# Optimization experiments

Measured on AMD Instinct MI355X. Metric: run time of the kernel, lower is better.

The kernel has to match this reference:

```python
import jax, jax.numpy as jnp
import numpy as np

N_NODES = 100000
N_EDGES = 1600000
IN_C = 128
HID_C = 64
HEADS = 2
OUT_C = 40
NEG_SLOPE = 0.2  # PyG GATConv default


def setup_inputs() -> dict:
    key = jax.random.key(0)
    ks = jax.random.split(key, 10)
    x = jax.random.normal(ks[0], (N_NODES, IN_C), dtype=jnp.float32)
    edge_index = jax.random.randint(ks[1], (2, N_EDGES), 0, N_NODES, dtype=jnp.int32)
    # layer 1 params: Linear(in, heads*hid), att_src/att_dst [heads, hid], bias [heads*hid]
    s1 = 1.0 / np.sqrt(IN_C)
    W1 = jax.random.uniform(ks[2], (IN_C, HEADS * HID_C), minval=-s1, maxval=s1, dtype=jnp.float32)
    att_src1 = jax.random.normal(ks[3], (HEADS, HID_C), dtype=jnp.float32) * 0.1
    att_dst1 = jax.random.normal(ks[4], (HEADS, HID_C), dtype=jnp.float32) * 0.1
    b1 = jnp.zeros((HEADS * HID_C,), dtype=jnp.float32)
    # layer 2 params: Linear(heads*hid, out), heads=1, concat=False
    s2 = 1.0 / np.sqrt(HEADS * HID_C)
    W2 = jax.random.uniform(ks[5], (HEADS * HID_C, OUT_C), minval=-s2, maxval=s2, dtype=jnp.float32)
    att_src2 = jax.random.normal(ks[6], (1, OUT_C), dtype=jnp.float32) * 0.1
    att_dst2 = jax.random.normal(ks[7], (1, OUT_C), dtype=jnp.float32) * 0.1
    b2 = jnp.zeros((OUT_C,), dtype=jnp.float32)
    return {"x": x, "edge_index": edge_index, "W1": W1, "att_src1": att_src1,
            "att_dst1": att_dst1, "b1": b1, "W2": W2, "att_src2": att_src2,
            "att_dst2": att_dst2, "b2": b2}


def _gat_conv(x, src, dst, n, W, a_src, a_dst):
    # x: [N, F_in]; W: [F_in, H*C]; a_src/a_dst: [H, C]
    H, C = a_src.shape
    h = (x @ W).reshape(n, H, C)                       # [N, H, C]
    alpha_src = jnp.einsum('nhc,hc->nh', h, a_src)     # [N, H]
    alpha_dst = jnp.einsum('nhc,hc->nh', h, a_dst)
    e = alpha_src[src] + alpha_dst[dst]                # [E, H]
    e = jax.nn.leaky_relu(e, NEG_SLOPE)
    # numerically stable softmax over edges grouped by destination node
    m = jax.ops.segment_max(e, dst, num_segments=n)    # [N, H]
    ex = jnp.exp(e - m[dst])
    s = jax.ops.segment_sum(ex, dst, num_segments=n)
    coef = ex / (s[dst] + 1e-16)                       # [E, H]
    msg = h[src] * coef[:, :, None]                    # [E, H, C]
    return jax.ops.segment_sum(msg, dst, num_segments=n)  # [N, H, C]


def reference(x, edge_index, W1, att_src1, att_dst1, b1, W2, att_src2, att_dst2, b2):
    n = x.shape[0]
    # PyG GATConv adds self-loops by default
    loops = jnp.arange(n, dtype=edge_index.dtype)
    src = jnp.concatenate([edge_index[0], loops])
    dst = jnp.concatenate([edge_index[1], loops])
    # layer 1: heads=2, concat -> [N, H*C] + bias, then ELU
    h1 = _gat_conv(x, src, dst, n, W1, att_src1, att_dst1)
    h1 = h1.reshape(n, -1) + b1
    h1 = jax.nn.elu(h1)
    # layer 2: heads=1, concat=False -> mean over heads (=squeeze) + bias
    h2 = _gat_conv(h1, src, dst, n, W2, att_src2, att_dst2)
    h2 = h2.mean(axis=1) + b2
    return jax.nn.log_softmax(h2, axis=1)
```

## Files before the change

kernel.cpp:

```cpp
#include <hip/hip_runtime.h>
#include <hip/hip_fp16.h>
#include <math.h>

#define N_NODES 100000
#define N_EDGES 1600000
#define E_TOT   (N_EDGES + N_NODES)

#define NB     512
#define NPB    196
#define BCAP   4096
#define BIN_CH 4096
#define NBIN_WG ((E_TOT + BIN_CH - 1) / BIN_CH)

__device__ __forceinline__ float wexp(float v) {
    v = v > 0.f ? v : 0.2f * v;
    return __expf(v);
}

__global__ __launch_bounds__(256) void gemm1_k(
    const float* __restrict__ x, const float* __restrict__ W1,
    const float* __restrict__ as1, const float* __restrict__ ad1,
    __half* __restrict__ h1h, float* __restrict__ asrc, float* __restrict__ adst)
{
    __shared__ float xs[64][65];
    __shared__ float Wsh[64][128];
    const int t = threadIdx.x;
    const int nbase = blockIdx.x * 64;
    const int c4 = t & 31;
    const int ng = t >> 5;

    float acc[8][4];
#pragma unroll
    for (int i = 0; i < 8; ++i)
#pragma unroll
        for (int j = 0; j < 4; ++j) acc[i][j] = 0.f;

    for (int kt = 0; kt < 128; kt += 64) {
        __syncthreads();
        {
            int r = t >> 4;
            int c = (t & 15) * 4;
#pragma unroll
            for (int p = 0; p < 4; ++p) {
                int row = p * 16 + r;
                int gr = nbase + row; if (gr > N_NODES - 1) gr = N_NODES - 1;
                float4 v = *(const float4*)(x + (size_t)gr * 128 + kt + c);
                xs[row][c + 0] = v.x; xs[row][c + 1] = v.y;
                xs[row][c + 2] = v.z; xs[row][c + 3] = v.w;
            }
        }
        {
            int r = t >> 5;
            int c = (t & 31) * 4;
#pragma unroll
            for (int p = 0; p < 8; ++p) {
                int row = p * 8 + r;
                *(float4*)&Wsh[row][c] = *(const float4*)(W1 + (size_t)(kt + row) * 128 + c);
            }
        }
        __syncthreads();

#pragma unroll 4
        for (int k = 0; k < 64; ++k) {
            float4 w = *(const float4*)&Wsh[k][c4 * 4];
            float x0 = xs[ng * 8 + 0][k], x1 = xs[ng * 8 + 1][k];
            float x2 = xs[ng * 8 + 2][k], x3 = xs[ng * 8 + 3][k];
            float x4 = xs[ng * 8 + 4][k], x5 = xs[ng * 8 + 5][k];
            float x6 = xs[ng * 8 + 6][k], x7 = xs[ng * 8 + 7][k];
            acc[0][0] += x0 * w.x; acc[0][1] += x0 * w.y; acc[0][2] += x0 * w.z; acc[0][3] += x0 * w.w;
            acc[1][0] += x1 * w.x; acc[1][1] += x1 * w.y; acc[1][2] += x1 * w.z; acc[1][3] += x1 * w.w;
            acc[2][0] += x2 * w.x; acc[2][1] += x2 * w.y; acc[2][2] += x2 * w.z; acc[2][3] += x2 * w.w;
            acc[3][0] += x3 * w.x; acc[3][1] += x3 * w.y; acc[3][2] += x3 * w.z; acc[3][3] += x3 * w.w;
            acc[4][0] += x4 * w.x; acc[4][1] += x4 * w.y; acc[4][2] += x4 * w.z; acc[4][3] += x4 * w.w;
            acc[5][0] += x5 * w.x; acc[5][1] += x5 * w.y; acc[5][2] += x5 * w.z; acc[5][3] += x5 * w.w;
            acc[6][0] += x6 * w.x; acc[6][1] += x6 * w.y; acc[6][2] += x6 * w.z; acc[6][3] += x6 * w.w;
            acc[7][0] += x7 * w.x; acc[7][1] += x7 * w.y; acc[7][2] += x7 * w.z; acc[7][3] += x7 * w.w;
        }
    }

    float4 as4 = ((const float4*)as1)[c4];
    float4 ad4 = ((const float4*)ad1)[c4];
#pragma unroll
    for (int i = 0; i < 8; ++i) {
        int node = nbase + ng * 8 + i;
        float ax = acc[i][0], ay = acc[i][1], az = acc[i][2], aw = acc[i][3];
        if (node < N_NODES) {
            __half2* row = (__half2*)(h1h + (size_t)node * 128);
            row[2 * c4]     = __floats2half2_rn(ax, ay);
            row[2 * c4 + 1] = __floats2half2_rn(az, aw);
        }
        float ps = ax * as4.x + ay * as4.y + az * as4.z + aw * as4.w;
        float pd = ax * ad4.x + ay * ad4.y + az * ad4.z + aw * ad4.w;
#pragma unroll
        for (int off = 1; off < 16; off <<= 1) {
            ps += __shfl_xor(ps, off);
            pd += __shfl_xor(pd, off);
        }
        if ((t & 15) == 0 && node < N_NODES) {
            int h = c4 >> 4;
            asrc[node * 2 + h] = ps;
            adst[node * 2 + h] = pd;
        }
    }
}

__global__ __launch_bounds__(256) void bin_k(
    const int* __restrict__ ei, int* __restrict__ bcur, unsigned* __restrict__ bdata)
{
    __shared__ int hist[NB];
    __shared__ int base[NB];
    const int t = threadIdx.x;
    const int e0 = blockIdx.x * BIN_CH;
    const int n = min(BIN_CH, E_TOT - e0);

    for (int b = t; b < NB; b += 256) hist[b] = 0;
    __syncthreads();

    for (int i = t; i < n; i += 256) {
        int e = e0 + i;
        int d = (e < N_EDGES) ? ei[N_EDGES + e] : e - N_EDGES;
        atomicAdd(&hist[d / NPB], 1);
    }
    __syncthreads();

    for (int b = t; b < NB; b += 256) {
        int c = hist[b];
        base[b] = c ? atomicAdd(&bcur[b], c) : 0;
        hist[b] = 0;
    }
    __syncthreads();

    for (int i = t; i < n; i += 256) {
        int e = e0 + i;
        int s, d;
        if (e < N_EDGES) { s = ei[e]; d = ei[N_EDGES + e]; }
        else             { s = d = e - N_EDGES; }
        int b  = d / NPB;
        int dl = d - b * NPB;
        int pos = base[b] + atomicAdd(&hist[b], 1);
        if (pos < BCAP)
            bdata[(size_t)b * BCAP + pos] = (unsigned)s | ((unsigned)dl << 17);
    }
}

__global__ __launch_bounds__(512) void scanb_k(
    const int* __restrict__ bcur, int* __restrict__ bbase)
{
    __shared__ int a[NB], b_[NB];
    int t = threadIdx.x;
    int v = bcur[t];
    a[t] = v;
    __syncthreads();
    int* src = a; int* dst = b_;
    for (int off = 1; off < NB; off <<= 1) {
        dst[t] = (t >= off) ? src[t - off] + src[t] : src[t];
        __syncthreads();
        int* tmp = src; src = dst; dst = tmp;
    }
    bbase[t] = src[t] - v;
}

__global__ __launch_bounds__(256) void build_k(
    const unsigned* __restrict__ bdata, const int* __restrict__ bcur,
    const int* __restrict__ bbase, int* __restrict__ row_start,
    int* __restrict__ csr_src)
{
    __shared__ unsigned rec[BCAP];
    __shared__ int hist[256];
    __shared__ int excl[NPB];
    __shared__ int lcur[NPB];
    const int t = threadIdx.x;
    const int b = blockIdx.x;
    const int cnt = min(bcur[b], BCAP);
    const int bb = bbase[b];

    hist[t] = 0;
    if (t < NPB) lcur[t] = 0;
    __syncthreads();

    for (int i = t; i < cnt; i += 256) {
        unsigned r = bdata[(size_t)b * BCAP + i];
        rec[i] = r;
        atomicAdd(&hist[r >> 17], 1);
    }
    __syncthreads();

    int v = hist[t];
    __syncthreads();
    for (int off = 1; off < 256; off <<= 1) {
        int y = (t >= off) ? hist[t - off] : 0;
        __syncthreads();
        hist[t] += y;
        __syncthreads();
    }
    if (t < NPB) excl[t] = hist[t] - v;
    __syncthreads();

    int node = b * NPB + t;
    if (t < NPB && node <= N_NODES) row_start[node] = bb + excl[t];

    for (int i = t; i < cnt; i += 256) {
        unsigned r = rec[i];
        int dl = r >> 17;
        int s  = r & 0x1FFFF;
        int slot = atomicAdd(&lcur[dl], 1);
        csr_src[bb + excl[dl] + slot] = s;
    }
}

__global__ __launch_bounds__(256) void fagg1_k(
    const int* __restrict__ csr_src, const int* __restrict__ row_start,
    const float* __restrict__ asrc, const float* __restrict__ adst,
    const __half* __restrict__ h1h, const float* __restrict__ b1,
    __half* __restrict__ out1h)
{
    int node = blockIdx.x * 4 + (threadIdx.x >> 6);
    int L = threadIdx.x & 63;
    int h = L >> 5;
    int b = row_start[node], e = row_start[node + 1];
    const float* as_h = asrc + h;
    float ad = adst[node * 2 + h];
    const __half2* H = (const __half2*)h1h;

    float2 a0 = make_float2(0.f, 0.f), a1 = a0, a2 = a0, a3 = a0;
    float d0 = 0.f, d1 = 0.f, d2 = 0.f, d3 = 0.f;

    int j = b;
    for (; j + 3 < e; j += 4) {
        int s0 = csr_src[j], s1 = csr_src[j + 1], s2 = csr_src[j + 2], s3 = csr_src[j + 3];
        float w0 = wexp(as_h[s0 * 2] + ad);
        float w1 = wexp(as_h[s1 * 2] + ad);
        float w2 = wexp(as_h[s2 * 2] + ad);
        float w3 = wexp(as_h[s3 * 2] + ad);
        float2 x0 = __half22float2(H[(size_t)s0 * 64 + L]);
        float2 x1 = __half22float2(H[(size_t)s1 * 64 + L]);
        float2 x2 = __half22float2(H[(size_t)s2 * 64 + L]);
        float2 x3 = __half22float2(H[(size_t)s3 * 64 + L]);
        a0.x += w0 * x0.x; a0.y += w0 * x0.y; d0 += w0;
        a1.x += w1 * x1.x; a1.y += w1 * x1.y; d1 += w1;
        a2.x += w2 * x2.x; a2.y += w2 * x2.y; d2 += w2;
        a3.x += w3 * x3.x; a3.y += w3 * x3.y; d3 += w3;
    }
    for (; j < e; ++j) {
        int s = csr_src[j];
        float w = wexp(as_h[s * 2] + ad);
        float2 xv = __half22float2(H[(size_t)s * 64 + L]);
        a0.x += w * xv.x; a0.y += w * xv.y; d0 += w;
    }

    float inv = 1.f / (((d0 + d1) + (d2 + d3)) + 1e-16f);
    float2 bb = ((const float2*)b1)[L];
    float vx = (a0.x + a1.x + a2.x + a3.x) * inv + bb.x;
    float vy = (a0.y + a1.y + a2.y + a3.y) * inv + bb.y;
    vx = vx > 0.f ? vx : expm1f(vx);
    vy = vy > 0.f ? vy : expm1f(vy);
    ((__half2*)(out1h + (size_t)node * 128))[L] = __floats2half2_rn(vx, vy);
}

__global__ __launch_bounds__(256) void gemm2_k(
    const __half* __restrict__ in1h, const float* __restrict__ W2,
    const float* __restrict__ as2, const float* __restrict__ ad2,
    __half* __restrict__ h2h, float* __restrict__ asrc, float* __restrict__ adst)
{
    __shared__ float xs[64][65];
    __shared__ float Wsh[64][64];
    __shared__ float as_s[64], ad_s[64];
    const int t = threadIdx.x;
    const int nbase = blockIdx.x * 64;
    const int c4 = t & 15;
    const int ng = t >> 4;

    if (t < 64) {
        as_s[t] = (t < 40) ? as2[t] : 0.f;
        ad_s[t] = (t < 40) ? ad2[t] : 0.f;
    }

    float acc[4][4];
#pragma unroll
    for (int i = 0; i < 4; ++i)
#pragma unroll
        for (int j = 0; j < 4; ++j) acc[i][j] = 0.f;

    for (int kt = 0; kt < 128; kt += 64) {
        __syncthreads();
        {
            int r = t >> 4;
            int c = (t & 15) * 4;
#pragma unroll
            for (int p = 0; p < 4; ++p) {
                int row = p * 16 + r;
                int gr = nbase + row; if (gr > N_NODES - 1) gr = N_NODES - 1;
                const __half2* src = (const __half2*)(in1h + (size_t)gr * 128 + kt + c);
                float2 f01 = __half22float2(src[0]);
                float2 f23 = __half22float2(src[1]);
                xs[row][c + 0] = f01.x; xs[row][c + 1] = f01.y;
                xs[row][c + 2] = f23.x; xs[row][c + 3] = f23.y;
            }
        }
        for (int i = t; i < 4096; i += 256) {
            int k = i >> 6, c = i & 63;
            Wsh[k][c] = (c < 40) ? W2[(size_t)(kt + k) * 40 + c] : 0.f;
        }
        __syncthreads();

#pragma unroll 4
        for (int k = 0; k < 64; ++k) {
            float4 w = *(const float4*)&Wsh[k][c4 * 4];
            float x0 = xs[ng * 4 + 0][k], x1 = xs[ng * 4 + 1][k];
            float x2 = xs[ng * 4 + 2][k], x3 = xs[ng * 4 + 3][k];
            acc[0][0] += x0 * w.x; acc[0][1] += x0 * w.y; acc[0][2] += x0 * w.z; acc[0][3] += x0 * w.w;
            acc[1][0] += x1 * w.x; acc[1][1] += x1 * w.y; acc[1][2] += x1 * w.z; acc[1][3] += x1 * w.w;
            acc[2][0] += x2 * w.x; acc[2][1] += x2 * w.y; acc[2][2] += x2 * w.z; acc[2][3] += x2 * w.w;
            acc[3][0] += x3 * w.x; acc[3][1] += x3 * w.y; acc[3][2] += x3 * w.z; acc[3][3] += x3 * w.w;
        }
    }

    float4 as4 = *(const float4*)&as_s[c4 * 4];
    float4 ad4 = *(const float4*)&ad_s[c4 * 4];
#pragma unroll
    for (int i = 0; i < 4; ++i) {
        int node = nbase + ng * 4 + i;
        float ax = acc[i][0], ay = acc[i][1], az = acc[i][2], aw = acc[i][3];
        if (node < N_NODES) {
            __half2* row = (__half2*)(h2h + (size_t)node * 64);
            row[2 * c4]     = __floats2half2_rn(ax, ay);
            row[2 * c4 + 1] = __floats2half2_rn(az, aw);
        }
        float ps = ax * as4.x + ay * as4.y + az * as4.z + aw * as4.w;
        float pd = ax * ad4.x + ay * ad4.y + az * ad4.z + aw * ad4.w;
#pragma unroll
        for (int off = 1; off < 16; off <<= 1) {
            ps += __shfl_xor(ps, off);
            pd += __shfl_xor(pd, off);
        }
        if ((t & 15) == 0 && node < N_NODES) {
            asrc[node] = ps;
            adst[node] = pd;
        }
    }
}

__global__ __launch_bounds__(256) void fagg2_k(
    const int* __restrict__ csr_src, const int* __restrict__ row_start,
    const float* __restrict__ asrc, const float* __restrict__ adst,
    const __half* __restrict__ h2h, const float* __restrict__ b2,
    float* __restrict__ out)
{
    int node = blockIdx.x * 4 + (threadIdx.x >> 6);
    int L = threadIdx.x & 63;
    bool act = L < 40;
    int col = act ? L : 0;
    int b = row_start[node], e = row_start[node + 1];
    float ad = adst[node];

    float a0 = 0.f, a1 = 0.f, a2 = 0.f, a3 = 0.f;
    float d0 = 0.f, d1 = 0.f, d2 = 0.f, d3 = 0.f;

    int j = b;
    for (; j + 3 < e; j += 4) {
        int s0 = csr_src[j], s1 = csr_src[j + 1], s2 = csr_src[j + 2], s3 = csr_src[j + 3];
        float w0 = wexp(asrc[s0] + ad);
        float w1 = wexp(asrc[s1] + ad);
        float w2 = wexp(asrc[s2] + ad);
        float w3 = wexp(asrc[s3] + ad);
        float x0 = __half2float(h2h[(size_t)s0 * 64 + col]);
        float x1 = __half2float(h2h[(size_t)s1 * 64 + col]);
        float x2 = __half2float(h2h[(size_t)s2 * 64 + col]);
        float x3 = __half2float(h2h[(size_t)s3 * 64 + col]);
        a0 += w0 * x0; d0 += w0;
        a1 += w1 * x1; d1 += w1;
        a2 += w2 * x2; d2 += w2;
        a3 += w3 * x3; d3 += w3;
    }
    for (; j < e; ++j) {
        int s = csr_src[j];
        float w = wexp(asrc[s] + ad);
        float xv = __half2float(h2h[(size_t)s * 64 + col]);
        a0 += w * xv; d0 += w;
    }

    float den = (d0 + d1) + (d2 + d3);
    float acc = (a0 + a1) + (a2 + a3);
    float v = act ? acc / (den + 1e-16f) + b2[L] : -1e30f;
    float mx = v;
#pragma unroll
    for (int off = 32; off; off >>= 1) mx = fmaxf(mx, __shfl_xor(mx, off));
    float ex = act ? __expf(v - mx) : 0.f;
#pragma unroll
    for (int off = 32; off; off >>= 1) ex += __shfl_xor(ex, off);
    if (act) out[(size_t)node * 40 + L] = v - mx - logf(ex);
}

extern "C" void kernel_launch(void* const* d_in, const int* in_sizes, int n_in,
                              void* d_out, int out_size, void* d_ws, size_t ws_size,
                              hipStream_t stream)
{
    const float* x   = (const float*)d_in[0];
    const int*   ei  = (const int*)d_in[1];
    const float* W1  = (const float*)d_in[2];
    const float* as1 = (const float*)d_in[3];
    const float* ad1 = (const float*)d_in[4];
    const float* b1  = (const float*)d_in[5];
    const float* W2  = (const float*)d_in[6];
    const float* as2 = (const float*)d_in[7];
    const float* ad2 = (const float*)d_in[8];
    const float* b2  = (const float*)d_in[9];
    float* out = (float*)d_out;

    float* ws = (float*)d_ws;
    __half* h1h   = (__half*)ws;
    __half* out1h = (__half*)(ws + 6400000);
    float* asrc1 = ws + 19200000;
    float* adst1 = ws + 19400000;
    float* asrc2 = ws + 19600000;
    float* adst2 = ws + 19700000;
    int* bcur      = (int*)(ws + 19800000);
    int* bbase     = (int*)(ws + 19801000);
    int* row_start = (int*)(ws + 19802000);
    int* csr_src   = (int*)(ws + 19910000);
    unsigned* bdata = (unsigned*)(ws + 21700000);

    hipMemsetAsync(bcur, 0, NB * sizeof(int), stream);

    bin_k<<<NBIN_WG, 256, 0, stream>>>(ei, bcur, bdata);
    scanb_k<<<1, 512, 0, stream>>>(bcur, bbase);
    build_k<<<NB, 256, 0, stream>>>(bdata, bcur, bbase, row_start, csr_src);

    gemm1_k<<<1563, 256, 0, stream>>>(x, W1, as1, ad1, h1h, asrc1, adst1);
    fagg1_k<<<25000, 256, 0, stream>>>(csr_src, row_start, asrc1, adst1, h1h, b1, out1h);

    __half* h2h = h1h;
    gemm2_k<<<1563, 256, 0, stream>>>(out1h, W2, as2, ad2, h2h, asrc2, adst2);
    fagg2_k<<<25000, 256, 0, stream>>>(csr_src, row_start, asrc2, adst2, h2h, b2, out);
}
```

Measured before the change: 301.3 us.

## Precompute per-edge attention weights and denominators in separate edge kernels

Adds edge-weight kernels that compute the leaky-relu exp attention weight once per edge (and per head), store them in CSR order, and reduce per-node denominators. The aggregation kernels then read contiguous weights instead of gathering asrc and recomputing exp in every lane. This removes redundant per-lane exp and random asrc gathers, but adds two extra launches plus a write and re-read of the edge weight arrays. Workspace offsets are shifted to make room for the new buffers.

```diff
diff --git a/kernel.cpp b/kernel.cpp
--- a/kernel.cpp
+++ b/kernel.cpp
@@ -208,9 +208,54 @@
     }
 }
 
+__global__ __launch_bounds__(256) void edgew1_k(
+    const int* __restrict__ csr_src, const int* __restrict__ row_start,
+    const float2* __restrict__ asrc2, const float2* __restrict__ adst2,
+    float2* __restrict__ wn, float2* __restrict__ dsum)
+{
+    int node = blockIdx.x * 4 + (threadIdx.x >> 6);
+    int L = threadIdx.x & 63;
+    int b = row_start[node], e = row_start[node + 1];
+    float2 ad = adst2[node];
+    float s0 = 0.f, s1 = 0.f;
+    for (int j = b + L; j < e; j += 64) {
+        float2 av = asrc2[csr_src[j]];
+        float w0 = wexp(av.x + ad.x);
+        float w1 = wexp(av.y + ad.y);
+        wn[j] = make_float2(w0, w1);
+        s0 += w0; s1 += w1;
+    }
+#pragma unroll
+    for (int off = 32; off; off >>= 1) {
+        s0 += __shfl_xor(s0, off);
+        s1 += __shfl_xor(s1, off);
+    }
+    if (L == 0) dsum[node] = make_float2(s0, s1);
+}
+
+__global__ __launch_bounds__(256) void edgew2_k(
+    const int* __restrict__ csr_src, const int* __restrict__ row_start,
+    const float* __restrict__ asrc, const float* __restrict__ adst,
+    float* __restrict__ wn, float* __restrict__ dsum)
+{
+    int node = blockIdx.x * 4 + (threadIdx.x >> 6);
+    int L = threadIdx.x & 63;
+    int b = row_start[node], e = row_start[node + 1];
+    float ad = adst[node];
+    float s = 0.f;
+    for (int j = b + L; j < e; j += 64) {
+        float w = wexp(asrc[csr_src[j]] + ad);
+        wn[j] = w;
+        s += w;
+    }
+#pragma unroll
+    for (int off = 32; off; off >>= 1) s += __shfl_xor(s, off);
+    if (L == 0) dsum[node] = s;
+}
+
 __global__ __launch_bounds__(256) void fagg1_k(
     const int* __restrict__ csr_src, const int* __restrict__ row_start,
-    const float* __restrict__ asrc, const float* __restrict__ adst,
+    const float2* __restrict__ wn, const float2* __restrict__ dsum,
     const __half* __restrict__ h1h, const float* __restrict__ b1,
     __half* __restrict__ out1h)
 {
@@ -218,37 +263,37 @@
     int L = threadIdx.x & 63;
     int h = L >> 5;
     int b = row_start[node], e = row_start[node + 1];
-    const float* as_h = asrc + h;
-    float ad = adst[node * 2 + h];
     const __half2* H = (const __half2*)h1h;
 
     float2 a0 = make_float2(0.f, 0.f), a1 = a0, a2 = a0, a3 = a0;
-    float d0 = 0.f, d1 = 0.f, d2 = 0.f, d3 = 0.f;
 
     int j = b;
     for (; j + 3 < e; j += 4) {
         int s0 = csr_src[j], s1 = csr_src[j + 1], s2 = csr_src[j + 2], s3 = csr_src[j + 3];
-        float w0 = wexp(as_h[s0 * 2] + ad);
-        float w1 = wexp(as_h[s1 * 2] + ad);
-        float w2 = wexp(as_h[s2 * 2] + ad);
-        float w3 = wexp(as_h[s3 * 2] + ad);
+        float2 u0 = wn[j], u1 = wn[j + 1], u2 = wn[j + 2], u3 = wn[j + 3];
         float2 x0 = __half22float2(H[(size_t)s0 * 64 + L]);
         float2 x1 = __half22float2(H[(size_t)s1 * 64 + L]);
         float2 x2 = __half22float2(H[(size_t)s2 * 64 + L]);
         float2 x3 = __half22float2(H[(size_t)s3 * 64 + L]);
-        a0.x += w0 * x0.x; a0.y += w0 * x0.y; d0 += w0;
-        a1.x += w1 * x1.x; a1.y += w1 * x1.y; d1 += w1;
-        a2.x += w2 * x2.x; a2.y += w2 * x2.y; d2 += w2;
-        a3.x += w3 * x3.x; a3.y += w3 * x3.y; d3 += w3;
+        float w0 = h ? u0.y : u0.x;
+        float w1 = h ? u1.y : u1.x;
+        float w2 = h ? u2.y : u2.x;
+        float w3 = h ? u3.y : u3.x;
+        a0.x += w0 * x0.x; a0.y += w0 * x0.y;
+        a1.x += w1 * x1.x; a1.y += w1 * x1.y;
+        a2.x += w2 * x2.x; a2.y += w2 * x2.y;
+        a3.x += w3 * x3.x; a3.y += w3 * x3.y;
     }
     for (; j < e; ++j) {
         int s = csr_src[j];
-        float w = wexp(as_h[s * 2] + ad);
+        float2 u = wn[j];
+        float w = h ? u.y : u.x;
         float2 xv = __half22float2(H[(size_t)s * 64 + L]);
-        a0.x += w * xv.x; a0.y += w * xv.y; d0 += w;
-    }
-
-    float inv = 1.f / (((d0 + d1) + (d2 + d3)) + 1e-16f);
+        a0.x += w * xv.x; a0.y += w * xv.y;
+    }
+
+    float2 ds = dsum[node];
+    float inv = 1.f / ((h ? ds.y : ds.x) + 1e-16f);
     float2 bb = ((const float2*)b1)[L];
     float vx = (a0.x + a1.x + a2.x + a3.x) * inv + bb.x;
     float vy = (a0.y + a1.y + a2.y + a3.y) * inv + bb.y;
@@ -320,14 +365,14 @@
 #pragma unroll
     for (int i = 0; i < 4; ++i) {
         int node = nbase + ng * 4 + i;
-        float ax = acc[i][0], ay = acc[i][1], az = acc[i][2], aw = acc[i][3];
+        float axx = acc[i][0], ayy = acc[i][1], azz = acc[i][2], aww = acc[i][3];
         if (node < N_NODES) {
             __half2* row = (__half2*)(h2h + (size_t)node * 64);
-            row[2 * c4]     = __floats2half2_rn(ax, ay);
-            row[2 * c4 + 1] = __floats2half2_rn(az, aw);
-        }
-        float ps = ax * as4.x + ay * as4.y + az * as4.z + aw * as4.w;
-        float pd = ax * ad4.x + ay * ad4.y + az * ad4.z + aw * ad4.w;
+            row[2 * c4]     = __floats2half2_rn(axx, ayy);
+            row[2 * c4 + 1] = __floats2half2_rn(azz, aww);
+        }
+        float ps = axx * as4.x + ayy * as4.y + azz * as4.z + aww * as4.w;
+        float pd = axx * ad4.x + ayy * ad4.y + azz * ad4.z + aww * ad4.w;
 #pragma unroll
         for (int off = 1; off < 16; off <<= 1) {
             ps += __shfl_xor(ps, off);
@@ -342,7 +387,7 @@
 
 __global__ __launch_bounds__(256) void fagg2_k(
     const int* __restrict__ csr_src, const int* __restrict__ row_start,
-    const float* __restrict__ asrc, const float* __restrict__ adst,
+    const float* __restrict__ wn, const float* __restrict__ dsum,
     const __half* __restrict__ h2h, const float* __restrict__ b2,
     float* __restrict__ out)
 {
@@ -351,35 +396,30 @@
     bool act = L < 40;
     int col = act ? L : 0;
     int b = row_start[node], e = row_start[node + 1];
-    float ad = adst[node];
 
     float a0 = 0.f, a1 = 0.f, a2 = 0.f, a3 = 0.f;
-    float d0 = 0.f, d1 = 0.f, d2 = 0.f, d3 = 0.f;
 
     int j = b;
     for (; j + 3 < e; j += 4) {
         int s0 = csr_src[j], s1 = csr_src[j + 1], s2 = csr_src[j + 2], s3 = csr_src[j + 3];
-        float w0 = wexp(asrc[s0] + ad);
-        float w1 = wexp(asrc[s1] + ad);
-        float w2 = wexp(asrc[s2] + ad);
-        float w3 = wexp(asrc[s3] + ad);
+        float w0 = wn[j], w1 = wn[j + 1], w2 = wn[j + 2], w3 = wn[j + 3];
         float x0 = __half2float(h2h[(size_t)s0 * 64 + col]);
         float x1 = __half2float(h2h[(size_t)s1 * 64 + col]);
         float x2 = __half2float(h2h[(size_t)s2 * 64 + col]);
         float x3 = __half2float(h2h[(size_t)s3 * 64 + col]);
-        a0 += w0 * x0; d0 += w0;
-        a1 += w1 * x1; d1 += w1;
-        a2 += w2 * x2; d2 += w2;
-        a3 += w3 * x3; d3 += w3;
+        a0 += w0 * x0;
+        a1 += w1 * x1;
+        a2 += w2 * x2;
+        a3 += w3 * x3;
     }
     for (; j < e; ++j) {
         int s = csr_src[j];
-        float w = wexp(asrc[s] + ad);
+        float w = wn[j];
         float xv = __half2float(h2h[(size_t)s * 64 + col]);
-        a0 += w * xv; d0 += w;
-    }
-
-    float den = (d0 + d1) + (d2 + d3);
+        a0 += w * xv;
+    }
+
+    float den = dsum[node];
     float acc = (a0 + a1) + (a2 + a3);
     float v = act ? acc / (den + 1e-16f) + b2[L] : -1e30f;
     float mx = v;
@@ -414,11 +454,15 @@
     float* adst1 = ws + 19400000;
     float* asrc2 = ws + 19600000;
     float* adst2 = ws + 19700000;
-    int* bcur      = (int*)(ws + 19800000);
-    int* bbase     = (int*)(ws + 19801000);
-    int* row_start = (int*)(ws + 19802000);
-    int* csr_src   = (int*)(ws + 19910000);
-    unsigned* bdata = (unsigned*)(ws + 21700000);
+    float* dsum1 = ws + 19810000;
+    float* dsum2 = ws + 20010000;
+    int* bcur      = (int*)(ws + 20110000);
+    int* bbase     = (int*)(ws + 20111000);
+    int* row_start = (int*)(ws + 20112000);
+    int* csr_src   = (int*)(ws + 20220000);
+    unsigned* bdata = (unsigned*)(ws + 22000000);
+    float* wn1     = ws + 24100000;
+    float* wn2     = wn1;
 
     hipMemsetAsync(bcur, 0, NB * sizeof(int), stream);
 
@@ -427,9 +471,15 @@
     build_k<<<NB, 256, 0, stream>>>(bdata, bcur, bbase, row_start, csr_src);
 
     gemm1_k<<<1563, 256, 0, stream>>>(x, W1, as1, ad1, h1h, asrc1, adst1);
-    fagg1_k<<<25000, 256, 0, stream>>>(csr_src, row_start, asrc1, adst1, h1h, b1, out1h);
+    edgew1_k<<<25000, 256, 0, stream>>>(csr_src, row_start,
+                                        (const float2*)asrc1, (const float2*)adst1,
+                                        (float2*)wn1, (float2*)dsum1);
+    fagg1_k<<<25000, 256, 0, stream>>>(csr_src, row_start,
+                                       (const float2*)wn1, (const float2*)dsum1,
+                                       h1h, b1, out1h);
 
     __half* h2h = h1h;
     gemm2_k<<<1563, 256, 0, stream>>>(out1h, W2, as2, ad2, h2h, asrc2, adst2);
-    fagg2_k<<<25000, 256, 0, stream>>>(csr_src, row_start, asrc2, adst2, h2h, b2, out);
-}
+    edgew2_k<<<25000, 256, 0, stream>>>(csr_src, row_start, asrc2, adst2, wn2, dsum2);
+    fagg2_k<<<25000, 256, 0, stream>>>(csr_src, row_start, wn2, dsum2, h2h, b2, out);
+}
```

Result: slower. 342.7 us (+13.7%).
